# Kernel optimization log

Measured on AMD Instinct MI355X. Metric: run time of the kernel, lower is better.

The kernel has to match this reference:

```python
import jax, jax.numpy as jnp
import numpy as np

N = 50000          # nodes
E = 800000         # edges
F = 128            # input features
H = 4              # heads
C = 16             # out_channels per head (h_dim // 2)
HC = H * C         # 64, concatenated hidden size
G = 128            # graphs in batch
NCLS = 10


def _lin(key, fan_in, fan_out):
    kw, kb = jax.random.split(key)
    scale = 1.0 / np.sqrt(fan_in)
    W = jax.random.uniform(kw, (fan_in, fan_out), minval=-scale, maxval=scale, dtype=jnp.float32)
    b = jax.random.uniform(kb, (fan_out,), minval=-scale, maxval=scale, dtype=jnp.float32)
    return W, b


def setup_inputs() -> dict:
    key = jax.random.key(0)
    ks = jax.random.split(key, 20)
    inp = {
        'x': jax.random.normal(ks[0], (N, F), dtype=jnp.float32),
        'edge_index': jax.random.randint(ks[1], (2, E), 0, N, dtype=jnp.int32),
        'batch_mapping': jnp.sort(jax.random.randint(ks[2], (N,), 0, G, dtype=jnp.int32)),
    }
    fan_ins = [F, HC, HC]
    ki = 3
    for layer, fin in enumerate(fan_ins, start=1):
        for nm in ('Wq', 'Wk', 'Wv', 'Ws'):
            Wmat, bvec = _lin(ks[ki], fin, HC); ki += 1
            inp[f'{nm}{layer}'] = Wmat
            inp[f'b{nm[1]}{layer}'] = bvec
    Wl, bl = _lin(ks[ki], HC, NCLS)
    inp['W_lin'] = Wl
    inp['b_lin'] = bl
    return inp


def _transformer_conv(x, src, dst, Wq, bq, Wk, bk, Wv, bv, Ws, bs):
    n = x.shape[0]
    q = (x @ Wq + bq).reshape(n, H, C)   # [N,H,C]
    k = (x @ Wk + bk).reshape(n, H, C)
    v = (x @ Wv + bv).reshape(n, H, C)
    # per-edge attention scores, softmax-normalized per destination node
    score = jnp.einsum('ehc,ehc->eh', q[dst], k[src]) / jnp.sqrt(jnp.asarray(C, x.dtype))  # [E,H]
    m = jax.ops.segment_max(score, dst, num_segments=n)          # [N,H]
    p = jnp.exp(score - m[dst])                                   # [E,H]
    denom = jax.ops.segment_sum(p, dst, num_segments=n)           # [N,H]
    alpha = p / (denom[dst] + 1e-16)
    agg = jax.ops.segment_sum(alpha[:, :, None] * v[src], dst, num_segments=n)  # [N,H,C]
    return agg.reshape(n, HC) + x @ Ws + bs  # root/skip connection


def reference(x, edge_index, batch_mapping,
              Wq1, bq1, Wk1, bk1, Wv1, bv1, Ws1, bs1,
              Wq2, bq2, Wk2, bk2, Wv2, bv2, Ws2, bs2,
              Wq3, bq3, Wk3, bk3, Wv3, bv3, Ws3, bs3,
              W_lin, b_lin):
    src, dst = edge_index[0], edge_index[1]
    h = jax.nn.relu(_transformer_conv(x, src, dst, Wq1, bq1, Wk1, bk1, Wv1, bv1, Ws1, bs1))
    h = jax.nn.relu(_transformer_conv(h, src, dst, Wq2, bq2, Wk2, bk2, Wv2, bv2, Ws2, bs2))
    h = _transformer_conv(h, src, dst, Wq3, bq3, Wk3, bk3, Wv3, bv3, Ws3, bs3)
    # global mean pool per graph
    counts = jax.ops.segment_sum(jnp.ones((h.shape[0],), h.dtype), batch_mapping, num_segments=G)
    pooled = jax.ops.segment_sum(h, batch_mapping, num_segments=G) / jnp.maximum(counts, 1.0)[:, None]
    logits = pooled @ W_lin + b_lin
    return jax.nn.softmax(logits, axis=1)
```

## Files before the change

### kernel.cpp

```cpp
#include <hip/hip_runtime.h>
#include <hip/hip_fp16.h>
#include <math.h>

#define N_NODES 50000
#define NPAD    50048
#define N_EDGES 800000
#define F_IN    128
#define HC      64
#define NG      128
#define NCLS    10
#define NXT     782
#define XCHUNK  98
#define DRANGE  6250
#define SCB     2048
#define MAXDEG  64

typedef __attribute__((ext_vector_type(8))) _Float16 f16x8;
typedef __attribute__((ext_vector_type(4))) float f32x4;
typedef _Float16 half2v __attribute__((ext_vector_type(2)));

__device__ __forceinline__ float fdot2_acc(unsigned a, unsigned b, float c) {
#if __has_builtin(__builtin_amdgcn_fdot2)
    half2v ha, hb;
    __builtin_memcpy(&ha, &a, 4);
    __builtin_memcpy(&hb, &b, 4);
    return __builtin_amdgcn_fdot2(ha, hb, c, false);
#else
    __half2 ha = *(__half2*)&a, hb = *(__half2*)&b;
    return c + __low2float(ha) * __low2float(hb) + __high2float(ha) * __high2float(hb);
#endif
}

__device__ __forceinline__ void ell_body(int bid, const int* __restrict__ src,
                                         const int* __restrict__ dst,
                                         int* __restrict__ deg,
                                         int* __restrict__ slots) {
    int grp = bid & 7;
    int nb = SCB >> 3;
    int slot = bid >> 3;
    int lo = grp * DRANGE, hi = lo + DRANGE;
    const int4* d4p = (const int4*)dst;
    const int4* s4p = (const int4*)src;
    int nchunks = N_EDGES >> 2;
    for (int t = slot * 256 + (int)threadIdx.x; t < nchunks; t += nb * 256) {
        int4 d = d4p[t];
        bool v0 = (d.x >= lo && d.x < hi);
        bool v1 = (d.y >= lo && d.y < hi);
        bool v2 = (d.z >= lo && d.z < hi);
        bool v3 = (d.w >= lo && d.w < hi);
        if (!(v0 | v1 | v2 | v3)) continue;
        int4 s = s4p[t];
        if (v0) { int r = atomicAdd(&deg[d.x], 1); if (r < MAXDEG) slots[d.x * MAXDEG + r] = s.x; }
        if (v1) { int r = atomicAdd(&deg[d.y], 1); if (r < MAXDEG) slots[d.y * MAXDEG + r] = s.y; }
        if (v2) { int r = atomicAdd(&deg[d.z], 1); if (r < MAXDEG) slots[d.z * MAXDEG + r] = s.z; }
        if (v3) { int r = atomicAdd(&deg[d.w], 1); if (r < MAXDEG) slots[d.w * MAXDEG + r] = s.w; }
    }
}

__global__ __launch_bounds__(256) void ellconv_kernel(
    const int* __restrict__ src, const int* __restrict__ dst,
    int* __restrict__ deg, int* __restrict__ slots,
    const float* __restrict__ x, unsigned short* __restrict__ xf16, int n4x,
    const float* __restrict__ W10, const float* __restrict__ W11,
    const float* __restrict__ W12, const float* __restrict__ W13,
    const float* __restrict__ W20, const float* __restrict__ W21,
    const float* __restrict__ W22, const float* __restrict__ W23,
    const float* __restrict__ W30, const float* __restrict__ W31,
    const float* __restrict__ W32, const float* __restrict__ W33,
    unsigned short* __restrict__ wt_h)
{
    int bid = blockIdx.x;
    if (bid < SCB) {
        ell_body(bid, src, dst, deg, slots);
    } else if (bid < SCB + 256) {
        int idx = (bid - SCB) * 256 + threadIdx.x;
        const float* W;
        int K, dbase, rr;
        if (idx < 32768) {
            int mat = idx >> 13; rr = idx & 8191; K = 128;
            W = (mat == 0) ? W10 : (mat == 1) ? W11 : (mat == 2) ? W12 : W13;
            dbase = 0 * 32768 + mat * 8192;
        } else if (idx < 49152) {
            int i2 = idx - 32768;
            int mat = i2 >> 12; rr = i2 & 4095; K = 64;
            W = (mat == 0) ? W20 : (mat == 1) ? W21 : (mat == 2) ? W22 : W23;
            dbase = 1 * 32768 + mat * 4096;
        } else {
            int i3 = idx - 49152;
            int mat = i3 >> 12; rr = i3 & 4095; K = 64;
            W = (mat == 0) ? W30 : (mat == 1) ? W31 : (mat == 2) ? W32 : W33;
            dbase = 2 * 32768 + mat * 4096;
        }
        int k = rr >> 6, c = rr & 63;
        float f = W[k * 64 + c];
        wt_h[dbase + c * K + k] = __half_as_ushort(__float2half_rn(f));
    } else {
        int t = (bid - SCB - 256) * 256 + threadIdx.x;
        if (t < n4x) {
            float4 f = ((const float4*)x)[t];
            ushort4 u;
            u.x = __half_as_ushort(__float2half_rn(f.x));
            u.y = __half_as_ushort(__float2half_rn(f.y));
            u.z = __half_as_ushort(__float2half_rn(f.z));
            u.w = __half_as_ushort(__float2half_rn(f.w));
            ((ushort4*)xf16)[t] = u;
        }
    }
}

__device__ __forceinline__ void gemm_epilogue(int y, int row0, int w, int lr, int kq,
    f32x4* acc,
    const float* __restrict__ b0, const float* __restrict__ b1,
    const float* __restrict__ b2, const float* __restrict__ b3,
    unsigned short* __restrict__ qp16, unsigned short* __restrict__ sf16,
    unsigned short* __restrict__ kvpk, int M)
{
    const float* bias = (y == 0) ? b0 : (y == 1) ? b1 : (y == 2) ? b2 : b3;
    if (y == 0 || y == 3) {
        unsigned short* dstp = (y == 0) ? qp16 : sf16;
        #pragma unroll
        for (int f = 0; f < 4; ++f) {
            float bv = bias[f * 16 + lr];
            #pragma unroll
            for (int r = 0; r < 4; ++r) {
                int gr = row0 + w * 16 + kq * 4 + r;
                if (gr < M)
                    dstp[(size_t)gr * 64 + f * 16 + lr] =
                        __half_as_ushort(__float2half_rn(acc[f][r] + bv));
            }
        }
    } else {
        int off = (y == 1) ? 0 : 64;
        #pragma unroll
        for (int f = 0; f < 4; ++f) {
            float bv = bias[f * 16 + lr];
            #pragma unroll
            for (int r = 0; r < 4; ++r) {
                int gr = row0 + w * 16 + kq * 4 + r;
                if (gr < M)
                    kvpk[(size_t)gr * 128 + off + f * 16 + lr] =
                        __half_as_ushort(__float2half_rn(acc[f][r] + bv));
            }
        }
    }
}

__global__ __launch_bounds__(256) void mfma_gemm_kernel(
    const unsigned short* __restrict__ A16, const unsigned short* __restrict__ Wt_h,
    const float* __restrict__ b0, const float* __restrict__ b1,
    const float* __restrict__ b2, const float* __restrict__ b3,
    unsigned short* __restrict__ qp16, unsigned short* __restrict__ sf16,
    unsigned short* __restrict__ kvpk, int M, int K)
{
    extern __shared__ char smem[];
    int bid = blockIdx.x;
    int xcd = bid & 7;
    int slot = bid >> 3;
    int xt = xcd * XCHUNK + (slot >> 2);
    int y = slot & 3;
    if (xt >= NXT) return;
    int row0 = xt * 64;

    const int tileB = 64 * K * 2;
    char* sA  = smem;
    char* sBh = smem + tileB;

    int tid = threadIdx.x;
    int cpr = K >> 3;
    int total = 64 * cpr;
    const f16x8* gA  = (const f16x8*)(A16 + (size_t)row0 * K);
    const f16x8* gBh = (const f16x8*)(Wt_h + (size_t)y * 64 * K);
    for (int t = tid; t < total; t += 256) {
        int row = t / cpr, cs = t - row * cpr;
        int dstB = row * (K * 2) + ((cs * 16) ^ ((row & 7) << 4));
        *(f16x8*)(sA + dstB)  = gA[t];
        *(f16x8*)(sBh + dstB) = gBh[t];
    }
    __syncthreads();

    int w = tid >> 6, lane = tid & 63, lr = lane & 15, kq = lane >> 4;
    f32x4 acc[4];
    #pragma unroll
    for (int f = 0; f < 4; ++f) acc[f] = (f32x4){0.f, 0.f, 0.f, 0.f};

    int arow = w * 16 + lr;
    int abase = arow * (K * 2);
    int aswz = (arow & 7) << 4;
    for (int ks = 0; ks < K; ks += 32) {
        int kb = ks * 2 + kq * 16;
        f16x8 a = *(const f16x8*)(sA + abase + (kb ^ aswz));
        #pragma unroll
        for (int f = 0; f < 4; ++f) {
            int brow = f * 16 + lr;
            int boff = brow * (K * 2) + (kb ^ ((brow & 7) << 4));
            f16x8 bh = *(const f16x8*)(sBh + boff);
            acc[f] = __builtin_amdgcn_mfma_f32_16x16x32_f16(a, bh, acc[f], 0, 0, 0);
        }
    }
    gemm_epilogue(y, row0, w, lr, kq, acc, b0, b1, b2, b3, qp16, sf16, kvpk, M);
}

__global__ __launch_bounds__(256) void attn_kernel(
    const unsigned short* __restrict__ qp, const unsigned short* __restrict__ sf16,
    const uint4* __restrict__ kv4,
    const int* __restrict__ deg, const int* __restrict__ slots,
    float* __restrict__ hout,
    unsigned short* __restrict__ h16,
    int n, int mode)
{
    __shared__ float lds[4][64 * 17];
    int node = (int)((blockIdx.x * (size_t)blockDim.x + threadIdx.x) >> 6);
    int lane = threadIdx.x & 63;
    int wl = threadIdx.x >> 6;
    if (node >= n) return;
    int h = lane >> 4, j = lane & 15;

    const uint4* q4 = (const uint4*)(qp + (size_t)node * 64 + h * 16);
    uint4 qa = q4[0], qb = q4[1];

    int dg = deg[node];
    if (dg > MAXDEG) dg = MAXDEG;
    const int* row = slots + (size_t)node * MAXDEG;
    float acc[16];
    #pragma unroll
    for (int c = 0; c < 16; ++c) acc[c] = 0.f;
    float dsum = 0.f;

    for (int eb = 0; eb < dg; eb += 16) {
        int e = eb + j;
        if (e < dg) {
            int src = row[e];
            const uint4* kvr = kv4 + (size_t)src * 16 + h * 2;
            uint4 ka = kvr[0], kb = kvr[1];
            uint4 va = kvr[8], vb = kvr[9];
            float s = 0.f;
            s = fdot2_acc(qa.x, ka.x, s);
            s = fdot2_acc(qa.y, ka.y, s);
            s = fdot2_acc(qa.z, ka.z, s);
            s = fdot2_acc(qa.w, ka.w, s);
            s = fdot2_acc(qb.x, kb.x, s);
            s = fdot2_acc(qb.y, kb.y, s);
            s = fdot2_acc(qb.z, kb.z, s);
            s = fdot2_acc(qb.w, kb.w, s);
            float p = __expf(s * 0.25f);
            dsum += p;
            unsigned uv[8] = {va.x, va.y, va.z, va.w, vb.x, vb.y, vb.z, vb.w};
            #pragma unroll
            for (int i = 0; i < 8; ++i) {
                __half2 hv = *(__half2*)&uv[i];
                acc[2 * i]     += p * __low2float(hv);
                acc[2 * i + 1] += p * __high2float(hv);
            }
        }
    }

    dsum += __shfl_xor(dsum, 1, 64);
    dsum += __shfl_xor(dsum, 2, 64);
    dsum += __shfl_xor(dsum, 4, 64);
    dsum += __shfl_xor(dsum, 8, 64);
    float inv = 1.f / (dsum + 1e-16f);

    float* L = lds[wl];
    int wb = lane * 17;
    #pragma unroll
    for (int c = 0; c < 16; ++c) L[wb + c] = acc[c];
    __builtin_amdgcn_wave_barrier();
    float sum = 0.f;
    int rb = (h * 16) * 17 + j;
    #pragma unroll
    for (int jj = 0; jj < 16; ++jj) sum += L[rb + jj * 17];

    float skip = __half2float(__ushort_as_half(sf16[(size_t)node * 64 + lane]));
    float outv = sum * inv + skip;
    if (mode == 1) {
        outv = fmaxf(outv, 0.f);
        h16[(size_t)node * 64 + lane] = __half_as_ushort(__float2half_rn(outv));
    } else {
        hout[(size_t)node * 64 + lane] = outv;
    }
}

__global__ __launch_bounds__(256) void poolhead_kernel(
    const float* __restrict__ h, const int* __restrict__ bm,
    const float* __restrict__ Wl, const float* __restrict__ bl,
    float* __restrict__ out)
{
    int g = blockIdx.x;
    int lo = 0, hi = N_NODES;
    while (lo < hi) { int mid = (lo + hi) >> 1; if (bm[mid] < g) lo = mid + 1; else hi = mid; }
    int s = lo;
    lo = 0; hi = N_NODES;
    while (lo < hi) { int mid = (lo + hi) >> 1; if (bm[mid] < g + 1) lo = mid + 1; else hi = mid; }
    int e = lo;

    int c = threadIdx.x & 63, sub = threadIdx.x >> 6;
    float sum = 0.f;
    for (int i = s + sub; i < e; i += 4) sum += h[(size_t)i * 64 + c];
    __shared__ float tmp[256];
    __shared__ float pl[64];
    tmp[threadIdx.x] = sum;
    __syncthreads();
    if (sub == 0) {
        sum = tmp[c] + tmp[c + 64] + tmp[c + 128] + tmp[c + 192];
        int cnt = e - s;
        pl[c] = sum / fmaxf((float)cnt, 1.0f);
    }
    __syncthreads();
    if (threadIdx.x < 64) {
        int lane = threadIdx.x;
        float logit = -INFINITY;
        if (lane < NCLS) {
            float acc = bl[lane];
            for (int k = 0; k < 64; ++k) acc += pl[k] * Wl[k * NCLS + lane];
            logit = acc;
        }
        float mx = logit;
        mx = fmaxf(mx, __shfl_xor(mx, 1, 64));
        mx = fmaxf(mx, __shfl_xor(mx, 2, 64));
        mx = fmaxf(mx, __shfl_xor(mx, 4, 64));
        mx = fmaxf(mx, __shfl_xor(mx, 8, 64));
        float ex = (lane < NCLS) ? __expf(logit - mx) : 0.f;
        float sm = ex;
        sm += __shfl_xor(sm, 1, 64);
        sm += __shfl_xor(sm, 2, 64);
        sm += __shfl_xor(sm, 4, 64);
        sm += __shfl_xor(sm, 8, 64);
        if (lane < NCLS) out[g * NCLS + lane] = ex / sm;
    }
}

extern "C" void kernel_launch(void* const* d_in, const int* in_sizes, int n_in,
                              void* d_out, int out_size, void* d_ws, size_t ws_size,
                              hipStream_t stream) {
    const float* x  = (const float*)d_in[0];
    const int*   ei = (const int*)d_in[1];
    const int*   bm = (const int*)d_in[2];
    const float* W1[4] = {(const float*)d_in[3], (const float*)d_in[5], (const float*)d_in[7], (const float*)d_in[9]};
    const float* B1[4] = {(const float*)d_in[4], (const float*)d_in[6], (const float*)d_in[8], (const float*)d_in[10]};
    const float* W2[4] = {(const float*)d_in[11], (const float*)d_in[13], (const float*)d_in[15], (const float*)d_in[17]};
    const float* B2[4] = {(const float*)d_in[12], (const float*)d_in[14], (const float*)d_in[16], (const float*)d_in[18]};
    const float* W3[4] = {(const float*)d_in[19], (const float*)d_in[21], (const float*)d_in[23], (const float*)d_in[25]};
    const float* B3[4] = {(const float*)d_in[20], (const float*)d_in[22], (const float*)d_in[24], (const float*)d_in[26]};
    const float* Wl = (const float*)d_in[27];
    const float* bl = (const float*)d_in[28];
    float* outp = (float*)d_out;

    float* hf     = (float*)d_ws;
    unsigned short* qp16 = (unsigned short*)(hf + (size_t)NPAD * 64);
    unsigned short* sf16 = qp16 + (size_t)NPAD * 64;
    unsigned short* kvpk = sf16 + (size_t)NPAD * 64;
    unsigned short* xf16 = kvpk + (size_t)NPAD * 128;
    unsigned short* hs16 = xf16 + (size_t)NPAD * 128;
    unsigned short* wt_h = hs16 + (size_t)NPAD * 64;
    int* deg     = (int*)(wt_h + 3 * 32768);
    int* slots   = deg + N_NODES;

    const int* srcp = ei;
    const int* dstp = ei + N_EDGES;

    int n4x = N_NODES * F_IN / 4;
    int ggrid = 8 * XCHUNK * 4;
    int agrid = (N_NODES + 3) / 4;
    size_t smem1  = (size_t)2 * 64 * F_IN * 2;
    size_t smem23 = (size_t)2 * 64 * HC * 2;

    hipMemsetAsync(deg, 0, N_NODES * sizeof(int), stream);

    int ecgrid = SCB + 256 + (n4x + 255) / 256;
    ellconv_kernel<<<ecgrid, 256, 0, stream>>>(
        srcp, dstp, deg, slots,
        x, xf16, n4x,
        W1[0], W1[1], W1[2], W1[3],
        W2[0], W2[1], W2[2], W2[3],
        W3[0], W3[1], W3[2], W3[3],
        wt_h);

    mfma_gemm_kernel<<<ggrid, 256, smem1, stream>>>(xf16,
        wt_h + 0 * 32768,
        B1[0], B1[1], B1[2], B1[3], qp16, sf16, kvpk, N_NODES, F_IN);
    attn_kernel<<<agrid, 256, 0, stream>>>(qp16, sf16, (const uint4*)kvpk, deg, slots,
                                           nullptr, hs16, N_NODES, 1);
    mfma_gemm_kernel<<<ggrid, 256, smem23, stream>>>(hs16,
        wt_h + 1 * 32768,
        B2[0], B2[1], B2[2], B2[3], qp16, sf16, kvpk, N_NODES, HC);
    attn_kernel<<<agrid, 256, 0, stream>>>(qp16, sf16, (const uint4*)kvpk, deg, slots,
                                           nullptr, hs16, N_NODES, 1);
    mfma_gemm_kernel<<<ggrid, 256, smem23, stream>>>(hs16,
        wt_h + 2 * 32768,
        B3[0], B3[1], B3[2], B3[3], qp16, sf16, kvpk, N_NODES, HC);
    attn_kernel<<<agrid, 256, 0, stream>>>(qp16, sf16, (const uint4*)kvpk, deg, slots,
                                           hf, nullptr, N_NODES, 0);

    poolhead_kernel<<<NG, 256, 0, stream>>>(hf, bm, Wl, bl, outp);
}
```

Baseline: 240.5 us.

## Reuse A tile across all four projections and pad degree counters

The GEMM kernel now loads each 64-row A tile into shared memory once and loops over the four weight matrices (Q, K, V, skip), instead of launching a separate block per projection that reloads the same A tile. Separately, per-node degree counters are spaced 16 ints apart so atomics on neighbouring nodes fall on different cache lines, reducing contention in the ELL build. The GEMM trade-off is a quarter as many blocks, each doing serialized work with extra barriers, which lowers parallelism. Padding multiplies the memset size and makes the degree reads in the attention kernel strided.

```diff
diff --git a/kernel.cpp b/kernel.cpp
--- a/kernel.cpp
+++ b/kernel.cpp
@@ -14,6 +14,7 @@
 #define DRANGE  6250
 #define SCB     2048
 #define MAXDEG  64
+#define DPAD    16
 
 typedef __attribute__((ext_vector_type(8))) _Float16 f16x8;
 typedef __attribute__((ext_vector_type(4))) float f32x4;
@@ -33,7 +34,7 @@
 
 __device__ __forceinline__ void ell_body(int bid, const int* __restrict__ src,
                                          const int* __restrict__ dst,
-                                         int* __restrict__ deg,
+                                         int* __restrict__ deg_p,
                                          int* __restrict__ slots) {
     int grp = bid & 7;
     int nb = SCB >> 3;
@@ -50,16 +51,16 @@
         bool v3 = (d.w >= lo && d.w < hi);
         if (!(v0 | v1 | v2 | v3)) continue;
         int4 s = s4p[t];
-        if (v0) { int r = atomicAdd(&deg[d.x], 1); if (r < MAXDEG) slots[d.x * MAXDEG + r] = s.x; }
-        if (v1) { int r = atomicAdd(&deg[d.y], 1); if (r < MAXDEG) slots[d.y * MAXDEG + r] = s.y; }
-        if (v2) { int r = atomicAdd(&deg[d.z], 1); if (r < MAXDEG) slots[d.z * MAXDEG + r] = s.z; }
-        if (v3) { int r = atomicAdd(&deg[d.w], 1); if (r < MAXDEG) slots[d.w * MAXDEG + r] = s.w; }
+        if (v0) { int r = atomicAdd(&deg_p[d.x * DPAD], 1); if (r < MAXDEG) slots[d.x * MAXDEG + r] = s.x; }
+        if (v1) { int r = atomicAdd(&deg_p[d.y * DPAD], 1); if (r < MAXDEG) slots[d.y * MAXDEG + r] = s.y; }
+        if (v2) { int r = atomicAdd(&deg_p[d.z * DPAD], 1); if (r < MAXDEG) slots[d.z * MAXDEG + r] = s.z; }
+        if (v3) { int r = atomicAdd(&deg_p[d.w * DPAD], 1); if (r < MAXDEG) slots[d.w * MAXDEG + r] = s.w; }
     }
 }
 
 __global__ __launch_bounds__(256) void ellconv_kernel(
     const int* __restrict__ src, const int* __restrict__ dst,
-    int* __restrict__ deg, int* __restrict__ slots,
+    int* __restrict__ deg_p, int* __restrict__ slots,
     const float* __restrict__ x, unsigned short* __restrict__ xf16, int n4x,
     const float* __restrict__ W10, const float* __restrict__ W11,
     const float* __restrict__ W12, const float* __restrict__ W13,
@@ -71,7 +72,7 @@
 {
     int bid = blockIdx.x;
     if (bid < SCB) {
-        ell_body(bid, src, dst, deg, slots);
+        ell_body(bid, src, dst, deg_p, slots);
     } else if (bid < SCB + 256) {
         int idx = (bid - SCB) * 256 + threadIdx.x;
         const float* W;
@@ -108,43 +109,6 @@
     }
 }
 
-__device__ __forceinline__ void gemm_epilogue(int y, int row0, int w, int lr, int kq,
-    f32x4* acc,
-    const float* __restrict__ b0, const float* __restrict__ b1,
-    const float* __restrict__ b2, const float* __restrict__ b3,
-    unsigned short* __restrict__ qp16, unsigned short* __restrict__ sf16,
-    unsigned short* __restrict__ kvpk, int M)
-{
-    const float* bias = (y == 0) ? b0 : (y == 1) ? b1 : (y == 2) ? b2 : b3;
-    if (y == 0 || y == 3) {
-        unsigned short* dstp = (y == 0) ? qp16 : sf16;
-        #pragma unroll
-        for (int f = 0; f < 4; ++f) {
-            float bv = bias[f * 16 + lr];
-            #pragma unroll
-            for (int r = 0; r < 4; ++r) {
-                int gr = row0 + w * 16 + kq * 4 + r;
-                if (gr < M)
-                    dstp[(size_t)gr * 64 + f * 16 + lr] =
-                        __half_as_ushort(__float2half_rn(acc[f][r] + bv));
-            }
-        }
-    } else {
-        int off = (y == 1) ? 0 : 64;
-        #pragma unroll
-        for (int f = 0; f < 4; ++f) {
-            float bv = bias[f * 16 + lr];
-            #pragma unroll
-            for (int r = 0; r < 4; ++r) {
-                int gr = row0 + w * 16 + kq * 4 + r;
-                if (gr < M)
-                    kvpk[(size_t)gr * 128 + off + f * 16 + lr] =
-                        __half_as_ushort(__float2half_rn(acc[f][r] + bv));
-            }
-        }
-    }
-}
-
 __global__ __launch_bounds__(256) void mfma_gemm_kernel(
     const unsigned short* __restrict__ A16, const unsigned short* __restrict__ Wt_h,
     const float* __restrict__ b0, const float* __restrict__ b1,
@@ -156,54 +120,90 @@
     int bid = blockIdx.x;
     int xcd = bid & 7;
     int slot = bid >> 3;
-    int xt = xcd * XCHUNK + (slot >> 2);
-    int y = slot & 3;
+    int xt = xcd * XCHUNK + slot;
     if (xt >= NXT) return;
     int row0 = xt * 64;
 
     const int tileB = 64 * K * 2;
-    char* sA  = smem;
-    char* sBh = smem + tileB;
+    char* sA = smem;
+    char* sB = smem + tileB;
 
     int tid = threadIdx.x;
     int cpr = K >> 3;
     int total = 64 * cpr;
-    const f16x8* gA  = (const f16x8*)(A16 + (size_t)row0 * K);
-    const f16x8* gBh = (const f16x8*)(Wt_h + (size_t)y * 64 * K);
+
+    const f16x8* gA = (const f16x8*)(A16 + (size_t)row0 * K);
     for (int t = tid; t < total; t += 256) {
         int row = t / cpr, cs = t - row * cpr;
         int dstB = row * (K * 2) + ((cs * 16) ^ ((row & 7) << 4));
-        *(f16x8*)(sA + dstB)  = gA[t];
-        *(f16x8*)(sBh + dstB) = gBh[t];
-    }
-    __syncthreads();
+        *(f16x8*)(sA + dstB) = gA[t];
+    }
 
     int w = tid >> 6, lane = tid & 63, lr = lane & 15, kq = lane >> 4;
-    f32x4 acc[4];
-    #pragma unroll
-    for (int f = 0; f < 4; ++f) acc[f] = (f32x4){0.f, 0.f, 0.f, 0.f};
-
     int arow = w * 16 + lr;
     int abase = arow * (K * 2);
     int aswz = (arow & 7) << 4;
-    for (int ks = 0; ks < K; ks += 32) {
-        int kb = ks * 2 + kq * 16;
-        f16x8 a = *(const f16x8*)(sA + abase + (kb ^ aswz));
+
+    for (int y = 0; y < 4; ++y) {
+        const f16x8* gB = (const f16x8*)(Wt_h + (size_t)y * 64 * K);
+        for (int t = tid; t < total; t += 256) {
+            int row = t / cpr, cs = t - row * cpr;
+            int dstB = row * (K * 2) + ((cs * 16) ^ ((row & 7) << 4));
+            *(f16x8*)(sB + dstB) = gB[t];
+        }
+        __syncthreads();
+
+        f32x4 acc[4];
         #pragma unroll
-        for (int f = 0; f < 4; ++f) {
-            int brow = f * 16 + lr;
-            int boff = brow * (K * 2) + (kb ^ ((brow & 7) << 4));
-            f16x8 bh = *(const f16x8*)(sBh + boff);
-            acc[f] = __builtin_amdgcn_mfma_f32_16x16x32_f16(a, bh, acc[f], 0, 0, 0);
-        }
-    }
-    gemm_epilogue(y, row0, w, lr, kq, acc, b0, b1, b2, b3, qp16, sf16, kvpk, M);
+        for (int f = 0; f < 4; ++f) acc[f] = (f32x4){0.f, 0.f, 0.f, 0.f};
+        for (int ks = 0; ks < K; ks += 32) {
+            int kb = ks * 2 + kq * 16;
+            f16x8 a = *(const f16x8*)(sA + abase + (kb ^ aswz));
+            #pragma unroll
+            for (int f = 0; f < 4; ++f) {
+                int brow = f * 16 + lr;
+                int boff = brow * (K * 2) + (kb ^ ((brow & 7) << 4));
+                f16x8 bh = *(const f16x8*)(sB + boff);
+                acc[f] = __builtin_amdgcn_mfma_f32_16x16x32_f16(a, bh, acc[f], 0, 0, 0);
+            }
+        }
+
+        const float* bias = (y == 0) ? b0 : (y == 1) ? b1 : (y == 2) ? b2 : b3;
+        if (y == 0 || y == 3) {
+            unsigned short* dstp = (y == 0) ? qp16 : sf16;
+            #pragma unroll
+            for (int f = 0; f < 4; ++f) {
+                float bv = bias[f * 16 + lr];
+                #pragma unroll
+                for (int r = 0; r < 4; ++r) {
+                    int gr = row0 + w * 16 + kq * 4 + r;
+                    if (gr < M)
+                        dstp[(size_t)gr * 64 + f * 16 + lr] =
+                            __half_as_ushort(__float2half_rn(acc[f][r] + bv));
+                }
+            }
+        } else {
+            int off = (y == 1) ? 0 : 64;
+            #pragma unroll
+            for (int f = 0; f < 4; ++f) {
+                float bv = bias[f * 16 + lr];
+                #pragma unroll
+                for (int r = 0; r < 4; ++r) {
+                    int gr = row0 + w * 16 + kq * 4 + r;
+                    if (gr < M)
+                        kvpk[(size_t)gr * 128 + off + f * 16 + lr] =
+                            __half_as_ushort(__float2half_rn(acc[f][r] + bv));
+                }
+            }
+        }
+        __syncthreads();
+    }
 }
 
 __global__ __launch_bounds__(256) void attn_kernel(
     const unsigned short* __restrict__ qp, const unsigned short* __restrict__ sf16,
     const uint4* __restrict__ kv4,
-    const int* __restrict__ deg, const int* __restrict__ slots,
+    const int* __restrict__ deg_p, const int* __restrict__ slots,
     float* __restrict__ hout,
     unsigned short* __restrict__ h16,
     int n, int mode)
@@ -218,7 +218,7 @@
     const uint4* q4 = (const uint4*)(qp + (size_t)node * 64 + h * 16);
     uint4 qa = q4[0], qb = q4[1];
 
-    int dg = deg[node];
+    int dg = deg_p[node * DPAD];
     if (dg > MAXDEG) dg = MAXDEG;
     const int* row = slots + (size_t)node * MAXDEG;
     float acc[16];
@@ -352,23 +352,23 @@
     unsigned short* xf16 = kvpk + (size_t)NPAD * 128;
     unsigned short* hs16 = xf16 + (size_t)NPAD * 128;
     unsigned short* wt_h = hs16 + (size_t)NPAD * 64;
-    int* deg     = (int*)(wt_h + 3 * 32768);
-    int* slots   = deg + N_NODES;
+    int* deg_p   = (int*)(wt_h + 3 * 32768);
+    int* slots   = deg_p + (size_t)N_NODES * DPAD;
 
     const int* srcp = ei;
     const int* dstp = ei + N_EDGES;
 
     int n4x = N_NODES * F_IN / 4;
-    int ggrid = 8 * XCHUNK * 4;
+    int ggrid = 8 * XCHUNK;
     int agrid = (N_NODES + 3) / 4;
     size_t smem1  = (size_t)2 * 64 * F_IN * 2;
     size_t smem23 = (size_t)2 * 64 * HC * 2;
 
-    hipMemsetAsync(deg, 0, N_NODES * sizeof(int), stream);
+    hipMemsetAsync(deg_p, 0, (size_t)N_NODES * DPAD * sizeof(int), stream);
 
     int ecgrid = SCB + 256 + (n4x + 255) / 256;
     ellconv_kernel<<<ecgrid, 256, 0, stream>>>(
-        srcp, dstp, deg, slots,
+        srcp, dstp, deg_p, slots,
         x, xf16, n4x,
         W1[0], W1[1], W1[2], W1[3],
         W2[0], W2[1], W2[2], W2[3],
@@ -378,17 +378,17 @@
     mfma_gemm_kernel<<<ggrid, 256, smem1, stream>>>(xf16,
         wt_h + 0 * 32768,
         B1[0], B1[1], B1[2], B1[3], qp16, sf16, kvpk, N_NODES, F_IN);
-    attn_kernel<<<agrid, 256, 0, stream>>>(qp16, sf16, (const uint4*)kvpk, deg, slots,
+    attn_kernel<<<agrid, 256, 0, stream>>>(qp16, sf16, (const uint4*)kvpk, deg_p, slots,
                                            nullptr, hs16, N_NODES, 1);
     mfma_gemm_kernel<<<ggrid, 256, smem23, stream>>>(hs16,
         wt_h + 1 * 32768,
         B2[0], B2[1], B2[2], B2[3], qp16, sf16, kvpk, N_NODES, HC);
-    attn_kernel<<<agrid, 256, 0, stream>>>(qp16, sf16, (const uint4*)kvpk, deg, slots,
+    attn_kernel<<<agrid, 256, 0, stream>>>(qp16, sf16, (const uint4*)kvpk, deg_p, slots,
                                            nullptr, hs16, N_NODES, 1);
     mfma_gemm_kernel<<<ggrid, 256, smem23, stream>>>(hs16,
         wt_h + 2 * 32768,
         B3[0], B3[1], B3[2], B3[3], qp16, sf16, kvpk, N_NODES, HC);
-    attn_kernel<<<agrid, 256, 0, stream>>>(qp16, sf16, (const uint4*)kvpk, deg, slots,
+    attn_kernel<<<agrid, 256, 0, stream>>>(qp16, sf16, (const uint4*)kvpk, deg_p, slots,
                                            hf, nullptr, N_NODES, 0);
 
     poolhead_kernel<<<NG, 256, 0, stream>>>(hf, bm, Wl, bl, outp);
```

After: 253.3 us. 5.4% more time.
